# Kernel optimization log

Hardware: AMD Instinct MI355X
Metric: run time of the kernel (lower is better)

The kernel has to match this reference:

```python
import jax, jax.numpy as jnp
import numpy as np

NEG_SLOPE = 0.01  # torch F.leaky_relu default
EPS = 1e-5        # torch BatchNorm default
N_HEADS = 8


def _bn(x, g, b):
    # BatchNorm3d in training mode: batch statistics over (N, D, H, W)
    mu = jnp.mean(x, axis=(0, 2, 3, 4), keepdims=True)
    var = jnp.var(x, axis=(0, 2, 3, 4), keepdims=True)
    xn = (x - mu) * jax.lax.rsqrt(var + EPS)
    return xn * g[None, :, None, None, None] + b[None, :, None, None, None]


def _leaky(x):
    return jnp.where(x >= 0, x, NEG_SLOPE * x)


def setup_inputs() -> dict:
    key = jax.random.key(0)
    ks = jax.random.split(key, 6)
    B, C, T, X, Y = 4, 64, 8, 96, 96
    s = 0.02
    return {
        "h": jax.random.normal(ks[0], (B, C, T, X, Y), jnp.float32),
        "conv0_w": jax.random.normal(ks[1], (C, C, 1, 3, 3), jnp.float32) * s,
        "conv0_b": jnp.zeros((C,), jnp.float32),
        "bn0_g": jnp.ones((C,), jnp.float32),
        "bn0_b": jnp.zeros((C,), jnp.float32),
        "bn1_g": jnp.ones((C,), jnp.float32),
        "bn1_b": jnp.zeros((C,), jnp.float32),
        "in_proj_w": jax.random.normal(ks[2], (3 * C, C), jnp.float32) * s,
        "in_proj_b": jnp.zeros((3 * C,), jnp.float32),
        "out_proj_w": jax.random.normal(ks[3], (C, C), jnp.float32) * s,
        "out_proj_b": jnp.zeros((C,), jnp.float32),
        "conv1_w": jax.random.normal(ks[4], (25, C), jnp.float32) * s,  # Conv1d k=1, squeezed
        "conv1_b": jnp.zeros((25,), jnp.float32),
    }


def reference(h, conv0_w, conv0_b, bn0_g, bn0_b, bn1_g, bn1_b,
              in_proj_w, in_proj_b, out_proj_w, out_proj_b, conv1_w, conv1_b):
    B, C, T, X, Y = h.shape
    H = N_HEADS
    Dh = C // H
    h_in = h

    # conv0: Conv3d kernel [1,3,3], padding [0,1,1]
    x = jax.lax.conv_general_dilated(
        h, conv0_w, window_strides=(1, 1, 1),
        padding=[(0, 0), (1, 1), (1, 1)],
        dimension_numbers=("NCDHW", "OIDHW", "NCDHW"))
    x = x + conv0_b[None, :, None, None, None]
    x = _leaky(_bn(x, bn0_g, bn0_b))

    # self-attention over the T axis; batch = B*X*Y, embed = C (torch to_mha layout)
    seq = jnp.transpose(x, (2, 0, 3, 4, 1)).reshape(T, B * X * Y, C)  # [T, N, C]
    qkv = seq @ in_proj_w.T + in_proj_b
    q, k, v = jnp.split(qkv, 3, axis=-1)
    scale = 1.0 / np.sqrt(Dh)
    q = q.reshape(T, -1, H, Dh) * jnp.asarray(scale, q.dtype)
    k = k.reshape(T, -1, H, Dh)
    v = v.reshape(T, -1, H, Dh)
    attn = jax.nn.softmax(jnp.einsum("qnhd,knhd->nhqk", q, k), axis=-1)
    o = jnp.einsum("nhqk,knhd->qnhd", attn, v).reshape(T, -1, C)
    o = o @ out_proj_w.T + out_proj_b
    # from_mha: [T, B, X, Y, C] -> [B, C, T, X, Y]
    o = jnp.transpose(o.reshape(T, B, X, Y, C), (1, 4, 0, 2, 3))

    x = _leaky(_bn(x + o, bn1_g, bn1_b))

    # spatial mean + 1x1 Conv1d -> per-(b,t) 5x5 kernels
    m = jnp.mean(x, axis=(3, 4))                                   # [B, C, T]
    kern = jnp.einsum("bct,oc->bot", m, conv1_w) + conv1_b[None, :, None]  # [B, 25, T]
    w = jnp.transpose(kern, (0, 2, 1)).reshape(B * T, 1, 5, 5)

    # dynamic depthwise conv: each (b,t) kernel applied across all C slices of h_in
    lhs = jnp.transpose(h_in, (1, 0, 2, 3, 4)).reshape(C, B * T, X, Y)  # N=C, channels=B*T
    out = jax.lax.conv_general_dilated(
        lhs, w, window_strides=(1, 1), padding=[(2, 2), (2, 2)],
        dimension_numbers=("NCHW", "OIHW", "NCHW"),
        feature_group_count=B * T)
    out = jnp.transpose(out.reshape(C, B, T, X, Y), (1, 0, 2, 3, 4))
    return out
```

## Files before the change

### kernel.cpp

```cpp
#include <hip/hip_runtime.h>
#include <hip/hip_bf16.h>

typedef __attribute__((ext_vector_type(8))) short  short8;
typedef __attribute__((ext_vector_type(4))) short  short4v;
typedef __attribute__((ext_vector_type(4))) float  floatx4;
typedef unsigned short ushort_t;
typedef __attribute__((ext_vector_type(4))) unsigned short ushort4v;
typedef __attribute__((ext_vector_type(8))) unsigned short ushort8v;

constexpr int B_=4, C_=64, T_=8, X_=96, Y_=96;
constexpr int XY_  = X_*Y_;
constexpr int TOT_ = B_*C_*T_*XY_;
constexpr float EPS_   = 1e-5f;
constexpr float SLOPE_ = 0.01f;
constexpr float QSC_   = 0.35355339059327373f;
constexpr float INV_BN_ = 1.0f/294912.0f;
constexpr float INV_XY_ = 1.0f/9216.0f;

constexpr size_t OFF_HT   = 0;
constexpr size_t OFF_X0   = 37748736;
constexpr size_t OFF_X2   = OFF_X0 + (size_t)TOT_*2;
constexpr size_t OFF_WB   = OFF_X2 + (size_t)TOT_*2;
constexpr size_t OFF_QP   = OFF_WB + 73728;
constexpr size_t OFF_WP   = OFF_QP + 24576;
constexpr size_t OFF_SUM0 = OFF_WP + 8192;
constexpr size_t OFF_SQ0  = OFF_SUM0 + 256;
constexpr size_t OFF_SUM1 = OFF_SQ0 + 256;
constexpr size_t OFF_SQ1  = OFF_SUM1 + 256;
constexpr size_t OFF_M    = OFF_SQ1 + 256;
constexpr size_t ZBYTES   = 1024 + 8192;
constexpr size_t OFF_SC0  = OFF_M + 8192;
constexpr size_t OFF_SH0  = OFF_SC0 + 256;
constexpr size_t OFF_SC1  = OFF_SH0 + 256;
constexpr size_t OFF_SH1  = OFF_SC1 + 256;
constexpr size_t OFF_KERN = OFF_SH1 + 256;

__device__ __forceinline__ float leaky_(float v){ return v >= 0.f ? v : SLOPE_*v; }
__device__ __forceinline__ float bf2f(ushort_t u){
    union { unsigned int i; float f; } c; c.i = ((unsigned int)u) << 16; return c.f;
}
__device__ __forceinline__ ushort_t f2bf(float f){
    __hip_bfloat16 b = __float2bfloat16(f);
    return *reinterpret_cast<ushort_t*>(&b);
}
__device__ __forceinline__ void s8f(short8 s, float* f){
    union { short8 s; unsigned int u[4]; } c; c.s = s;
    #pragma unroll
    for (int i=0;i<4;++i){
        union { unsigned int i; float f; } lo, hi;
        lo.i = c.u[i] << 16; hi.i = c.u[i] & 0xffff0000u;
        f[2*i] = lo.f; f[2*i+1] = hi.f;
    }
}

__global__ void k_prep(const float* __restrict__ w0, const float* __restrict__ wqkv,
                       const float* __restrict__ wo,
                       ushort_t* __restrict__ wB, short* __restrict__ qP, short* __restrict__ wP){
    int i = blockIdx.x*256 + threadIdx.x;
    if (i < 36864){
        int j = i & 7, lane = (i>>3) & 63, frag = i >> 9;
        int nt = frag & 3, kb = (frag>>2) & 1, tap = frag >> 3;
        int co = nt*16 + (lane & 15);
        int ci = kb*32 + (lane>>4)*8 + j;
        wB[i] = f2bf(w0[co*576 + ci*9 + tap]);
    } else if (i < 49152){
        int pos = i - 36864;
        int j = pos & 7, lane = (pos>>3)&63, kb = (pos>>9)&1, nt = pos>>10;
        int n = nt*16 + (lane&15);
        int c = kb*32 + (lane>>4)*8 + j;
        qP[pos] = (short)f2bf(wqkv[n*64 + c]);
    } else if (i < 53248){
        int pos = i - 49152;
        int j = pos & 7, lane = (pos>>3)&63, kb = (pos>>9)&1, nt = pos>>10;
        int n = nt*16 + (lane&15);
        int c = kb*32 + (lane>>4)*8 + j;
        wP[pos] = (short)f2bf(wo[n*64 + c]);
    }
}

__global__ __launch_bounds__(256) void k_hT(const float* __restrict__ h,
                                            ushort_t* __restrict__ hT){
    __shared__ float s[96*65];
    int x = blockIdx.x, bt = blockIdx.y;
    int b = bt >> 3, t = bt & 7;
    int c = threadIdx.x >> 2, yq = threadIdx.x & 3;
    const float* hp = h + ((size_t)(b*64 + c)*8 + t)*9216 + x*96 + yq*24;
    #pragma unroll
    for (int i=0;i<6;i++){
        float4 v = *(const float4*)(hp + i*4);
        int y = yq*24 + i*4;
        s[(y+0)*65 + c] = v.x;
        s[(y+1)*65 + c] = v.y;
        s[(y+2)*65 + c] = v.z;
        s[(y+3)*65 + c] = v.w;
    }
    __syncthreads();
    ushort_t* op = hT + ((size_t)(bt*96 + x)*96)*64;
    int o0 = threadIdx.x*24;
    #pragma unroll
    for (int v8=0; v8<3; ++v8){
        ushort8v pk;
        #pragma unroll
        for (int j=0;j<8;j++){
            int o = o0 + v8*8 + j;
            pk[j] = f2bf(s[(o>>6)*65 + (o&63)]);
        }
        *(ushort8v*)(op + o0 + v8*8) = pk;
    }
}

__global__ __launch_bounds__(256) void k_conv0(const ushort_t* __restrict__ hT,
        const ushort_t* __restrict__ wB, const float* __restrict__ bias,
        ushort_t* __restrict__ x0, float* __restrict__ sum0, float* __restrict__ sq0){
    __shared__ float red[512];
    int tid = threadIdx.x;
    int lane = tid & 63, w = tid >> 6;
    int m = lane & 15, q = lane >> 4;
    int bt = blockIdx.y, b = bt >> 3, t = bt & 7;
    int xr = blockIdx.x*4 + w;
    floatx4 acc[6][4];
    #pragma unroll
    for (int nt=0; nt<4; ++nt){
        float bv = bias[nt*16 + m];
        #pragma unroll
        for (int mt=0; mt<6; ++mt) acc[mt][nt] = {bv,bv,bv,bv};
    }
    const ushort_t* hbase = hT + (size_t)bt*589824;
    #pragma unroll
    for (int tap=0; tap<9; ++tap){
        int dx = tap/3, dy = tap%3;
        int xx = xr + dx - 1;
        if ((unsigned)xx >= 96u) continue;
        const ushort_t* hrow = hbase + (size_t)xx*6144 + q*8;
        #pragma unroll
        for (int kb=0; kb<2; ++kb){
            short8 bf[4];
            #pragma unroll
            for (int nt=0; nt<4; ++nt)
                bf[nt] = *(const short8*)(wB + ((tap*2+kb)*4 + nt)*512 + lane*8);
            #pragma unroll
            for (int mt=0; mt<6; ++mt){
                int y = mt*16 + m + dy - 1;
                short8 a = {0,0,0,0,0,0,0,0};
                if ((unsigned)y < 96u)
                    a = *(const short8*)(hrow + y*64 + kb*32);
                #pragma unroll
                for (int nt=0; nt<4; ++nt)
                    acc[mt][nt] = __builtin_amdgcn_mfma_f32_16x16x32_bf16(a, bf[nt], acc[mt][nt], 0,0,0);
            }
        }
    }
    float ls[4] = {0,0,0,0}, lq[4] = {0,0,0,0};
    size_t outb = ((size_t)(b*9216 + xr*96)*8 + t)*64;
    #pragma unroll
    for (int mt=0; mt<6; ++mt){
        #pragma unroll
        for (int nt=0; nt<4; ++nt){
            #pragma unroll
            for (int r=0; r<4; ++r){
                float v = acc[mt][nt][r];
                ls[nt] += v; lq[nt] += v*v;
                int y = mt*16 + q*4 + r;
                x0[outb + (size_t)y*512 + nt*16 + m] = f2bf(v);
            }
        }
    }
    #pragma unroll
    for (int nt=0; nt<4; ++nt){
        ls[nt] += __shfl_xor(ls[nt], 16); ls[nt] += __shfl_xor(ls[nt], 32);
        lq[nt] += __shfl_xor(lq[nt], 16); lq[nt] += __shfl_xor(lq[nt], 32);
    }
    if (lane < 16){
        #pragma unroll
        for (int nt=0; nt<4; ++nt){
            red[w*64 + nt*16 + lane]       = ls[nt];
            red[256 + w*64 + nt*16 + lane] = lq[nt];
        }
    }
    __syncthreads();
    if (tid < 64){
        float a  = red[tid] + red[64+tid] + red[128+tid] + red[192+tid];
        float qq = red[256+tid] + red[320+tid] + red[384+tid] + red[448+tid];
        atomicAdd(&sum0[tid], a);
        atomicAdd(&sq0[tid], qq);
    }
}

__global__ void k_fin(const float* __restrict__ sum, const float* __restrict__ sq,
                      const float* __restrict__ g, const float* __restrict__ be,
                      float* __restrict__ scale, float* __restrict__ shift, float inv_n){
    int c = threadIdx.x;
    float mu = sum[c]*inv_n;
    float var = sq[c]*inv_n - mu*mu;
    float rs = rsqrtf(var + EPS_);
    float sc = g[c]*rs;
    scale[c] = sc; shift[c] = be[c] - mu*sc;
}

__device__ __forceinline__ void attn_one(ushort_t* qs, const float* qf, int tok, int p, int h){
    int off_k = 64  + ((h ^ p)<<3);
    int off_v = 128 + ((h ^ p)<<3);
    float sv[8]; float mx = -1e30f;
    #pragma unroll
    for (int kt=0; kt<8; ++kt){
        short8 kv = *(const short8*)(qs + (p*8+kt)*200 + off_k);
        float kf[8]; s8f(kv, kf);
        float s = qf[0]*kf[0]+qf[1]*kf[1]+qf[2]*kf[2]+qf[3]*kf[3]
                + qf[4]*kf[4]+qf[5]*kf[5]+qf[6]*kf[6]+qf[7]*kf[7];
        sv[kt] = s; mx = fmaxf(mx, s);
    }
    float ssum = 0.f;
    #pragma unroll
    for (int kt=0;kt<8;++kt){ sv[kt] = __expf(sv[kt]-mx); ssum += sv[kt]; }
    float inv = 1.f/ssum;
    float o[8] = {0,0,0,0,0,0,0,0};
    #pragma unroll
    for (int kt=0;kt<8;++kt){
        short8 vv = *(const short8*)(qs + (p*8+kt)*200 + off_v);
        float vf[8]; s8f(vv, vf);
        #pragma unroll
        for (int j=0;j<8;++j) o[j] += sv[kt]*vf[j];
    }
    short8 ov;
    #pragma unroll
    for (int j=0;j<8;++j) ov[j] = (short)f2bf(o[j]*inv);
    *(short8*)(qs + tok*200 + h*8) = ov;
}

__global__ __launch_bounds__(256, 3) void k_attn(const ushort_t* __restrict__ x0,
        const float* __restrict__ sc0, const float* __restrict__ sh0,
        const short* __restrict__ qP, const float* __restrict__ bqkv,
        const short* __restrict__ wP, const float* __restrict__ bo,
        ushort_t* __restrict__ x2, float* __restrict__ sum1, float* __restrict__ sq1){
    __shared__ __align__(16) char smem[51200];
    ushort_t* qsA = (ushort_t*)smem;
    ushort_t* qsB = (ushort_t*)(smem + 25600);

    int tid = threadIdx.x;
    int b = blockIdx.z, xx = blockIdx.y, y0 = blockIdx.x*16;
    size_t slabA = ((size_t)(b*9216 + xx*96 + y0)) * 512;
    size_t slabB = slabA + 4096;

    int lane = tid & 63, w = tid >> 6;
    int c16 = lane & 15, qd = lane >> 4;

    {
        int tokA = w*16 + c16;
        const ushort_t* xrA = x0 + slabA + (size_t)tokA*64;
        const ushort_t* xrB = x0 + slabB + (size_t)tokA*64;
        ushort8v xaA = *(const ushort8v*)(xrA + qd*8);
        ushort8v xbA = *(const ushort8v*)(xrA + 32 + qd*8);
        ushort8v xaB = *(const ushort8v*)(xrB + qd*8);
        ushort8v xbB = *(const ushort8v*)(xrB + 32 + qd*8);
        float sca[8], sha[8], scb[8], shb[8];
        #pragma unroll
        for (int j=0;j<8;++j){
            sca[j] = sc0[qd*8 + j];      sha[j] = sh0[qd*8 + j];
            scb[j] = sc0[32 + qd*8 + j]; shb[j] = sh0[32 + qd*8 + j];
        }
        short8 a0A, a1A, a0B, a1B;
        #pragma unroll
        for (int j=0;j<8;++j){
            a0A[j] = (short)f2bf(leaky_(bf2f(xaA[j])*sca[j] + sha[j]));
            a1A[j] = (short)f2bf(leaky_(bf2f(xbA[j])*scb[j] + shb[j]));
            a0B[j] = (short)f2bf(leaky_(bf2f(xaB[j])*sca[j] + sha[j]));
            a1B[j] = (short)f2bf(leaky_(bf2f(xbB[j])*scb[j] + shb[j]));
        }
        #pragma unroll
        for (int nt=0; nt<12; ++nt){
            float bv = bqkv[nt*16 + c16];
            short8 b0 = *(const short8*)(qP + (nt*2+0)*512 + lane*8);
            short8 b1 = *(const short8*)(qP + (nt*2+1)*512 + lane*8);
            floatx4 accA = {bv,bv,bv,bv};
            floatx4 accB = {bv,bv,bv,bv};
            accA = __builtin_amdgcn_mfma_f32_16x16x32_bf16(a0A, b0, accA, 0, 0, 0);
            accB = __builtin_amdgcn_mfma_f32_16x16x32_bf16(a0B, b0, accB, 0, 0, 0);
            accA = __builtin_amdgcn_mfma_f32_16x16x32_bf16(a1A, b1, accA, 0, 0, 0);
            accB = __builtin_amdgcn_mfma_f32_16x16x32_bf16(a1B, b1, accB, 0, 0, 0);
            if (nt < 4){
                #pragma unroll
                for (int r=0;r<4;++r){ accA[r]*=QSC_; accB[r]*=QSC_; }
            }
            int c8 = nt*2 + (c16>>3);
            int sub = c16 & 7;
            #pragma unroll
            for (int r=0;r<4;++r){
                int row = w*16 + qd*4 + r;
                int p = row >> 3;
                qsA[row*200 + ((c8 ^ p)<<3) + sub] = f2bf(accA[r]);
                qsB[row*200 + ((c8 ^ p)<<3) + sub] = f2bf(accB[r]);
            }
        }
    }
    __syncthreads();

    {
        int tok = lane, p = tok >> 3;
        float qA0[8], qA1[8], qB0[8], qB1[8];
        short8 t0 = *(const short8*)(qsA + tok*200 + (((w  ) ^ p)<<3));
        short8 t1 = *(const short8*)(qsA + tok*200 + (((w+4) ^ p)<<3));
        short8 t2 = *(const short8*)(qsB + tok*200 + (((w  ) ^ p)<<3));
        short8 t3 = *(const short8*)(qsB + tok*200 + (((w+4) ^ p)<<3));
        s8f(t0, qA0); s8f(t1, qA1); s8f(t2, qB0); s8f(t3, qB1);
        attn_one(qsA, qA0, tok, p, w);
        attn_one(qsB, qB0, tok, p, w);
        attn_one(qsA, qA1, tok, p, w+4);
        attn_one(qsB, qB1, tok, p, w+4);
    }
    __syncthreads();

    {
        int row3 = w*16 + c16;
        short8 A0A = *(const short8*)(qsA + row3*200 + qd*8);
        short8 A1A = *(const short8*)(qsA + row3*200 + 32 + qd*8);
        short8 A0B = *(const short8*)(qsB + row3*200 + qd*8);
        short8 A1B = *(const short8*)(qsB + row3*200 + 32 + qd*8);
        #pragma unroll
        for (int nt=0; nt<4; ++nt){
            float bv = bo[nt*16 + c16];
            short8 b0 = *(const short8*)(wP + (nt*2+0)*512 + lane*8);
            short8 b1 = *(const short8*)(wP + (nt*2+1)*512 + lane*8);
            floatx4 accA = {bv,bv,bv,bv};
            floatx4 accB = {bv,bv,bv,bv};
            accA = __builtin_amdgcn_mfma_f32_16x16x32_bf16(A0A, b0, accA, 0, 0, 0);
            accB = __builtin_amdgcn_mfma_f32_16x16x32_bf16(A0B, b0, accB, 0, 0, 0);
            accA = __builtin_amdgcn_mfma_f32_16x16x32_bf16(A1A, b1, accA, 0, 0, 0);
            accB = __builtin_amdgcn_mfma_f32_16x16x32_bf16(A1B, b1, accB, 0, 0, 0);
            #pragma unroll
            for (int r=0;r<4;++r){
                int row = w*16 + qd*4 + r;
                qsA[row*200 + 64 + nt*16 + c16] = f2bf(accA[r]);
                qsB[row*200 + 64 + nt*16 + c16] = f2bf(accB[r]);
            }
        }
    }
    __syncthreads();

    float ls[4] = {0,0,0,0}, lq[4] = {0,0,0,0};
    #pragma unroll
    for (int it=0; it<4; ++it){
        int g = tid + it*256;
        int e0 = g*4, tk = g>>4, c0 = e0 & 63;
        floatx4 sc = *(const floatx4*)(sc0 + c0);
        floatx4 sh = *(const floatx4*)(sh0 + c0);
        ushort4v xvA = *(const ushort4v*)(x0 + slabA + e0);
        ushort4v xvB = *(const ushort4v*)(x0 + slabB + e0);
        short4v ovA = *(const short4v*)(qsA + tk*200 + 64 + c0);
        short4v ovB = *(const short4v*)(qsB + tk*200 + 64 + c0);
        ushort4v stA, stB;
        #pragma unroll
        for (int j=0;j<4;++j){
            float x1A = leaky_(bf2f(xvA[j])*sc[j] + sh[j]);
            float x1B = leaky_(bf2f(xvB[j])*sc[j] + sh[j]);
            stA[j] = f2bf(x1A + bf2f((ushort_t)ovA[j]));
            stB[j] = f2bf(x1B + bf2f((ushort_t)ovB[j]));
            float vA = bf2f(stA[j]), vB = bf2f(stB[j]);
            ls[j] += vA + vB; lq[j] += vA*vA + vB*vB;
        }
        *(ushort4v*)(x2 + slabA + e0) = stA;
        *(ushort4v*)(x2 + slabB + e0) = stB;
    }
    __syncthreads();
    float* red = (float*)smem;
    int slot = tid >> 4, c0s = (tid*4) & 63;
    #pragma unroll
    for (int j=0;j<4;++j){
        red[slot*64 + c0s + j]        = ls[j];
        red[1024 + slot*64 + c0s + j] = lq[j];
    }
    __syncthreads();
    if (tid < 128){
        int c = tid & 63;
        const float* base = red + (tid>>6)*1024 + c;
        float a = 0.f;
        #pragma unroll
        for (int s=0;s<16;++s) a += base[s*64];
        atomicAdd((tid < 64) ? &sum1[c] : &sq1[c], a);
    }
}

__global__ __launch_bounds__(256) void k_m(const ushort_t* __restrict__ x2,
        const float* __restrict__ sc1, const float* __restrict__ sh1,
        float* __restrict__ msum){
    __shared__ float sred[2048];
    int c = threadIdx.x & 63, tg = threadIdx.x >> 6;
    int b = blockIdx.y, chunk = blockIdx.x;
    float macc[8] = {0,0,0,0,0,0,0,0};
    float sc = sc1[c], sh = sh1[c];
    int xy_end = chunk*96 + 96;
    for (int xy = chunk*96 + tg; xy < xy_end; xy += 4){
        size_t base = ((size_t)(b*9216 + xy)*8)*64 + c;
        #pragma unroll
        for (int t=0;t<8;t++){
            float v = bf2f(x2[base + (size_t)t*64]);
            macc[t] += leaky_(v*sc + sh);
        }
    }
    #pragma unroll
    for (int t=0;t<8;t++) sred[tg*512 + t*64 + c] = macc[t];
    __syncthreads();
    #pragma unroll
    for (int i=0;i<2;++i){
        int idx = threadIdx.x + i*256;
        float a = sred[idx] + sred[512+idx] + sred[1024+idx] + sred[1536+idx];
        atomicAdd(&msum[b*512 + idx], a);
    }
}

__global__ void k_kern(const float* __restrict__ msum, const float* __restrict__ w1,
                       const float* __restrict__ b1, float* __restrict__ kern){
    int tid = blockIdx.x*256 + threadIdx.x;
    if (tid >= 800) return;
    int o = tid % 25; int t = (tid/25) % 8; int b = tid/200;
    float s = b1[o];
    const float* mrow = msum + (b*8+t)*64;
    for (int c=0;c<64;c++) s += (mrow[c]*INV_XY_) * w1[o*64+c];
    kern[(b*8+t)*25 + o] = s;
}

__global__ __launch_bounds__(256) void k_final(const float* __restrict__ h,
        const float* __restrict__ kern, float* __restrict__ out){
    __shared__ float s[100*104];
    int bct = blockIdx.x;
    int b = bct >> 9, t = bct & 7;
    int tid = threadIdx.x;
    const float* hp = h + (size_t)bct*9216;
    for (int i = tid; i < 1184; i += 256){
        int row, col;
        if (i < 416){ int r4 = i/104; row = (r4<2) ? r4 : 96 + r4; col = i - r4*104; }
        else { int j = i - 416; row = 2 + (j>>3); int k = j & 7; col = (k<4) ? k : 96 + k; }
        s[row*104 + col] = 0.f;
    }
    for (int i = tid; i < 2304; i += 256){
        int e = i*4; int xx = e/96, yy = e%96;
        float4 v = *(const float4*)(hp + e);
        *(float4*)(&s[(xx+2)*104 + yy + 4]) = v;
    }
    const float* kp = kern + ((size_t)(b*8+t))*25;
    float kv[25];
    #pragma unroll
    for (int i=0;i<25;i++) kv[i] = kp[i];
    __syncthreads();
    int tx = tid & 15, ty = tid >> 4;
    int x0 = ty*6, y0 = tx*6;
    float acc[6][6];
    #pragma unroll
    for (int i=0;i<6;i++)
        #pragma unroll
        for (int j=0;j<6;j++) acc[i][j] = 0.f;
    #pragma unroll
    for (int r=0; r<10; ++r){
        float row[10];
        const float* sp = &s[(x0+r)*104 + y0 + 2];
        #pragma unroll
        for (int c=0;c<10;c++) row[c] = sp[c];
        #pragma unroll
        for (int orow=0; orow<6; ++orow){
            if (orow > r || orow < r-4) continue;
            int dx = r - orow;
            #pragma unroll
            for (int dy=0; dy<5; ++dy){
                float wv = kv[dx*5+dy];
                #pragma unroll
                for (int oc=0; oc<6; ++oc)
                    acc[orow][oc] += wv * row[oc+dy];
            }
        }
    }
    float* op = out + (size_t)bct*9216 + x0*96 + y0;
    #pragma unroll
    for (int orow=0; orow<6; ++orow)
        #pragma unroll
        for (int oc=0; oc<6; ++oc)
            op[orow*96 + oc] = acc[orow][oc];
}

extern "C" void kernel_launch(void* const* d_in, const int* in_sizes, int n_in,
                              void* d_out, int out_size, void* d_ws, size_t ws_size,
                              hipStream_t stream){
    const float* h    = (const float*)d_in[0];
    const float* w0   = (const float*)d_in[1];
    const float* cb0  = (const float*)d_in[2];
    const float* bn0g = (const float*)d_in[3];
    const float* bn0b = (const float*)d_in[4];
    const float* bn1g = (const float*)d_in[5];
    const float* bn1b = (const float*)d_in[6];
    const float* wqkv = (const float*)d_in[7];
    const float* bqkv = (const float*)d_in[8];
    const float* wo   = (const float*)d_in[9];
    const float* bo   = (const float*)d_in[10];
    const float* w1   = (const float*)d_in[11];
    const float* b1   = (const float*)d_in[12];

    char* ws = (char*)d_ws;
    ushort_t* hT  = (ushort_t*)(ws + OFF_HT);
    ushort_t* x0  = (ushort_t*)(ws + OFF_X0);
    ushort_t* x2  = (ushort_t*)(ws + OFF_X2);
    ushort_t* wB  = (ushort_t*)(ws + OFF_WB);
    short* qP     = (short*)(ws + OFF_QP);
    short* wP     = (short*)(ws + OFF_WP);
    float* sum0   = (float*)(ws + OFF_SUM0);
    float* sq0    = (float*)(ws + OFF_SQ0);
    float* sum1   = (float*)(ws + OFF_SUM1);
    float* sq1    = (float*)(ws + OFF_SQ1);
    float* msum   = (float*)(ws + OFF_M);
    float* sc0    = (float*)(ws + OFF_SC0);
    float* sh0    = (float*)(ws + OFF_SH0);
    float* sc1    = (float*)(ws + OFF_SC1);
    float* sh1    = (float*)(ws + OFF_SH1);
    float* kern   = (float*)(ws + OFF_KERN);
    float* outp   = (float*)d_out;

    hipMemsetAsync(ws + OFF_SUM0, 0, ZBYTES, stream);
    k_prep  <<<208, 256, 0, stream>>>(w0, wqkv, wo, wB, qP, wP);
    k_hT    <<<dim3(96, 32), 256, 0, stream>>>(h, hT);
    k_conv0 <<<dim3(24, 32), 256, 0, stream>>>(hT, wB, cb0, x0, sum0, sq0);
    k_fin   <<<1, 64, 0, stream>>>(sum0, sq0, bn0g, bn0b, sc0, sh0, INV_BN_);
    k_attn  <<<dim3(6, 96, 4), 256, 0, stream>>>(x0, sc0, sh0, qP, bqkv, wP, bo, x2, sum1, sq1);
    k_fin   <<<1, 64, 0, stream>>>(sum1, sq1, bn1g, bn1b, sc1, sh1, INV_BN_);
    k_m     <<<dim3(96, 4), 256, 0, stream>>>(x2, sc1, sh1, msum);
    k_kern  <<<4, 256, 0, stream>>>(msum, w1, b1, kern);
    k_final <<<2048, 256, 0, stream>>>(h, kern, outp);
}
```

Measured before the change: 357.4 us.

## Pad hT rows with zero halo and split conv0 across y halves

The transposed bf16 input buffer gains a zero row at each end of every y line, so conv0 can drop its per-load y-bounds checks. conv0 now splits the 96 y positions into two halves via blockIdx.z, which halves its accumulator count and doubles the grid. It also adds a launch-bounds occupancy hint. The aim is more waves in flight and less branching in the MFMA loop, at the cost of a slightly larger hT buffer and x-tap loads repeated across both halves.

```diff
diff --git a/kernel.cpp b/kernel.cpp
--- a/kernel.cpp
+++ b/kernel.cpp
@@ -17,8 +17,13 @@
 constexpr float INV_BN_ = 1.0f/294912.0f;
 constexpr float INV_XY_ = 1.0f/9216.0f;
 
+constexpr int HT_ROWS_ = 98;
+constexpr int HT_XSTR_ = HT_ROWS_*64;
+constexpr int HT_BTSTR_ = 96*HT_XSTR_;
+constexpr size_t HT_BYTES_ = (size_t)32*HT_BTSTR_*2;
+
 constexpr size_t OFF_HT   = 0;
-constexpr size_t OFF_X0   = 37748736;
+constexpr size_t OFF_X0   = HT_BYTES_;
 constexpr size_t OFF_X2   = OFF_X0 + (size_t)TOT_*2;
 constexpr size_t OFF_WB   = OFF_X2 + (size_t)TOT_*2;
 constexpr size_t OFF_QP   = OFF_WB + 73728;
@@ -95,7 +100,14 @@
         s[(y+3)*65 + c] = v.w;
     }
     __syncthreads();
-    ushort_t* op = hT + ((size_t)(bt*96 + x)*96)*64;
+    ushort_t* opb = hT + (size_t)(bt*96 + x)*HT_XSTR_;
+    if (threadIdx.x < 16){
+        ushort8v z8 = {0,0,0,0,0,0,0,0};
+        int r = (threadIdx.x < 8) ? 0 : 97;
+        int o = (threadIdx.x & 7)*8;
+        *(ushort8v*)(opb + r*64 + o) = z8;
+    }
+    ushort_t* op = opb + 64;
     int o0 = threadIdx.x*24;
     #pragma unroll
     for (int v8=0; v8<3; ++v8){
@@ -109,7 +121,7 @@
     }
 }
 
-__global__ __launch_bounds__(256) void k_conv0(const ushort_t* __restrict__ hT,
+__global__ __launch_bounds__(256, 5) void k_conv0(const ushort_t* __restrict__ hT,
         const ushort_t* __restrict__ wB, const float* __restrict__ bias,
         ushort_t* __restrict__ x0, float* __restrict__ sum0, float* __restrict__ sq0){
     __shared__ float red[512];
@@ -118,20 +130,21 @@
     int m = lane & 15, q = lane >> 4;
     int bt = blockIdx.y, b = bt >> 3, t = bt & 7;
     int xr = blockIdx.x*4 + w;
-    floatx4 acc[6][4];
+    int z = blockIdx.z;
+    floatx4 acc[3][4];
     #pragma unroll
     for (int nt=0; nt<4; ++nt){
         float bv = bias[nt*16 + m];
         #pragma unroll
-        for (int mt=0; mt<6; ++mt) acc[mt][nt] = {bv,bv,bv,bv};
-    }
-    const ushort_t* hbase = hT + (size_t)bt*589824;
+        for (int mt=0; mt<3; ++mt) acc[mt][nt] = {bv,bv,bv,bv};
+    }
+    const ushort_t* hbase = hT + (size_t)bt*HT_BTSTR_;
     #pragma unroll
     for (int tap=0; tap<9; ++tap){
         int dx = tap/3, dy = tap%3;
         int xx = xr + dx - 1;
         if ((unsigned)xx >= 96u) continue;
-        const ushort_t* hrow = hbase + (size_t)xx*6144 + q*8;
+        const ushort_t* hrow = hbase + (size_t)xx*HT_XSTR_ + (z*48 + m + dy)*64 + q*8;
         #pragma unroll
         for (int kb=0; kb<2; ++kb){
             short8 bf[4];
@@ -139,11 +152,8 @@
             for (int nt=0; nt<4; ++nt)
                 bf[nt] = *(const short8*)(wB + ((tap*2+kb)*4 + nt)*512 + lane*8);
             #pragma unroll
-            for (int mt=0; mt<6; ++mt){
-                int y = mt*16 + m + dy - 1;
-                short8 a = {0,0,0,0,0,0,0,0};
-                if ((unsigned)y < 96u)
-                    a = *(const short8*)(hrow + y*64 + kb*32);
+            for (int mt=0; mt<3; ++mt){
+                short8 a = *(const short8*)(hrow + mt*1024 + kb*32);
                 #pragma unroll
                 for (int nt=0; nt<4; ++nt)
                     acc[mt][nt] = __builtin_amdgcn_mfma_f32_16x16x32_bf16(a, bf[nt], acc[mt][nt], 0,0,0);
@@ -153,14 +163,14 @@
     float ls[4] = {0,0,0,0}, lq[4] = {0,0,0,0};
     size_t outb = ((size_t)(b*9216 + xr*96)*8 + t)*64;
     #pragma unroll
-    for (int mt=0; mt<6; ++mt){
+    for (int mt=0; mt<3; ++mt){
         #pragma unroll
         for (int nt=0; nt<4; ++nt){
             #pragma unroll
             for (int r=0; r<4; ++r){
                 float v = acc[mt][nt][r];
                 ls[nt] += v; lq[nt] += v*v;
-                int y = mt*16 + q*4 + r;
+                int y = z*48 + mt*16 + q*4 + r;
                 x0[outb + (size_t)y*512 + nt*16 + m] = f2bf(v);
             }
         }
@@ -514,7 +524,7 @@
     hipMemsetAsync(ws + OFF_SUM0, 0, ZBYTES, stream);
     k_prep  <<<208, 256, 0, stream>>>(w0, wqkv, wo, wB, qP, wP);
     k_hT    <<<dim3(96, 32), 256, 0, stream>>>(h, hT);
-    k_conv0 <<<dim3(24, 32), 256, 0, stream>>>(hT, wB, cb0, x0, sum0, sq0);
+    k_conv0 <<<dim3(24, 32, 2), 256, 0, stream>>>(hT, wB, cb0, x0, sum0, sq0);
     k_fin   <<<1, 64, 0, stream>>>(sum0, sq0, bn0g, bn0b, sc0, sh0, INV_BN_);
     k_attn  <<<dim3(6, 96, 4), 256, 0, stream>>>(x0, sc0, sh0, qP, bqkv, wP, bo, x2, sum1, sq1);
     k_fin   <<<1, 64, 0, stream>>>(sum1, sq1, bn1g, bn1b, sc1, sh1, INV_BN_);
```

After: 367.1 us. 1.03x slower.

## Stage padded hT tile into LDS for conv0 with swizzled async loads

Applied to the files above, without the earlier changes.

The transposed input hT is now stored with a one-row, one-column zero halo (98x98 per bt), so conv0 no longer needs bounds checks. Each conv0 block copies its 6-row padded tile into LDS with global_load_lds and an XOR swizzle, then reads the A fragments for all nine taps from LDS instead of re-reading global memory. This is meant to cut redundant global and L2 traffic across taps. The cost is about 76KB of LDS per block, which limits occupancy to 2 blocks per CU, plus extra halo writes in k_hT.

```diff
diff --git a/kernel.cpp b/kernel.cpp
--- a/kernel.cpp
+++ b/kernel.cpp
@@ -17,8 +17,12 @@
 constexpr float INV_BN_ = 1.0f/294912.0f;
 constexpr float INV_XY_ = 1.0f/9216.0f;
 
+constexpr int HT_XSTR_  = 98*64;
+constexpr int HT_BTSTR_ = 98*HT_XSTR_;
+constexpr size_t HT_BYTES_ = (size_t)32*HT_BTSTR_*2;
+
 constexpr size_t OFF_HT   = 0;
-constexpr size_t OFF_X0   = 37748736;
+constexpr size_t OFF_X0   = HT_BYTES_ + 4096;
 constexpr size_t OFF_X2   = OFF_X0 + (size_t)TOT_*2;
 constexpr size_t OFF_WB   = OFF_X2 + (size_t)TOT_*2;
 constexpr size_t OFF_QP   = OFF_WB + 73728;
@@ -51,6 +55,11 @@
         lo.i = c.u[i] << 16; hi.i = c.u[i] & 0xffff0000u;
         f[2*i] = lo.f; f[2*i+1] = hi.f;
     }
+}
+__device__ __forceinline__ void gld16(const void* gp, void* lp){
+    __builtin_amdgcn_global_load_lds(
+        (const __attribute__((address_space(1))) void*)gp,
+        (__attribute__((address_space(3))) void*)lp, 16, 0, 0);
 }
 
 __global__ void k_prep(const float* __restrict__ w0, const float* __restrict__ wqkv,
@@ -81,8 +90,16 @@
 __global__ __launch_bounds__(256) void k_hT(const float* __restrict__ h,
                                             ushort_t* __restrict__ hT){
     __shared__ float s[96*65];
-    int x = blockIdx.x, bt = blockIdx.y;
+    int xp = blockIdx.x, bt = blockIdx.y;
     int b = bt >> 3, t = bt & 7;
+    ushort_t* opb = hT + (size_t)(bt*98 + xp)*HT_XSTR_;
+    if (xp == 0 || xp == 97){
+        ushort8v z8 = {0,0,0,0,0,0,0,0};
+        for (int i = threadIdx.x; i < 784; i += 256)
+            *(ushort8v*)(opb + i*8) = z8;
+        return;
+    }
+    int x = xp - 1;
     int c = threadIdx.x >> 2, yq = threadIdx.x & 3;
     const float* hp = h + ((size_t)(b*64 + c)*8 + t)*9216 + x*96 + yq*24;
     #pragma unroll
@@ -95,7 +112,13 @@
         s[(y+3)*65 + c] = v.w;
     }
     __syncthreads();
-    ushort_t* op = hT + ((size_t)(bt*96 + x)*96)*64;
+    if (threadIdx.x < 16){
+        ushort8v z8 = {0,0,0,0,0,0,0,0};
+        int r = (threadIdx.x < 8) ? 0 : 97;
+        int o = (threadIdx.x & 7)*8;
+        *(ushort8v*)(opb + r*64 + o) = z8;
+    }
+    ushort_t* op = opb + 64;
     int o0 = threadIdx.x*24;
     #pragma unroll
     for (int v8=0; v8<3; ++v8){
@@ -109,15 +132,27 @@
     }
 }
 
-__global__ __launch_bounds__(256) void k_conv0(const ushort_t* __restrict__ hT,
+__global__ __launch_bounds__(256, 2) void k_conv0(const ushort_t* __restrict__ hT,
         const ushort_t* __restrict__ wB, const float* __restrict__ bias,
         ushort_t* __restrict__ x0, float* __restrict__ sum0, float* __restrict__ sq0){
+    __shared__ __align__(16) char lds[77824];
     __shared__ float red[512];
     int tid = threadIdx.x;
     int lane = tid & 63, w = tid >> 6;
     int m = lane & 15, q = lane >> 4;
     int bt = blockIdx.y, b = bt >> 3, t = bt & 7;
-    int xr = blockIdx.x*4 + w;
+    int bx = blockIdx.x;
+    int xr = bx*4 + w;
+
+    {
+        const char* gsrc = (const char*)(hT + ((size_t)bt*98 + bx*4)*HT_XSTR_);
+        #pragma unroll
+        for (int it=0; it<19; ++it){
+            int lin = (tid + it*256)*16;
+            int src = lin ^ (((lin>>7)&7)<<4);
+            gld16(gsrc + src, lds + lin);
+        }
+    }
     floatx4 acc[6][4];
     #pragma unroll
     for (int nt=0; nt<4; ++nt){
@@ -125,25 +160,23 @@
         #pragma unroll
         for (int mt=0; mt<6; ++mt) acc[mt][nt] = {bv,bv,bv,bv};
     }
-    const ushort_t* hbase = hT + (size_t)bt*589824;
+    __syncthreads();
+
     #pragma unroll
     for (int tap=0; tap<9; ++tap){
-        int dx = tap/3, dy = tap%3;
-        int xx = xr + dx - 1;
-        if ((unsigned)xx >= 96u) continue;
-        const ushort_t* hrow = hbase + (size_t)xx*6144 + q*8;
+        const int dx = tap/3, dy = tap%3;
+        int rowg = (w + dx)*98 + m + dy;
+        int swz  = (rowg & 7) << 4;
         #pragma unroll
         for (int kb=0; kb<2; ++kb){
             short8 bf[4];
             #pragma unroll
             for (int nt=0; nt<4; ++nt)
                 bf[nt] = *(const short8*)(wB + ((tap*2+kb)*4 + nt)*512 + lane*8);
+            int va = (rowg*128 + kb*64 + q*16) ^ swz;
             #pragma unroll
             for (int mt=0; mt<6; ++mt){
-                int y = mt*16 + m + dy - 1;
-                short8 a = {0,0,0,0,0,0,0,0};
-                if ((unsigned)y < 96u)
-                    a = *(const short8*)(hrow + y*64 + kb*32);
+                short8 a = *(const short8*)(lds + va + mt*2048);
                 #pragma unroll
                 for (int nt=0; nt<4; ++nt)
                     acc[mt][nt] = __builtin_amdgcn_mfma_f32_16x16x32_bf16(a, bf[nt], acc[mt][nt], 0,0,0);
@@ -513,7 +546,7 @@
 
     hipMemsetAsync(ws + OFF_SUM0, 0, ZBYTES, stream);
     k_prep  <<<208, 256, 0, stream>>>(w0, wqkv, wo, wB, qP, wP);
-    k_hT    <<<dim3(96, 32), 256, 0, stream>>>(h, hT);
+    k_hT    <<<dim3(98, 32), 256, 0, stream>>>(h, hT);
     k_conv0 <<<dim3(24, 32), 256, 0, stream>>>(hT, wB, cb0, x0, sum0, sq0);
     k_fin   <<<1, 64, 0, stream>>>(sum0, sq0, bn0g, bn0b, sc0, sh0, INV_BN_);
     k_attn  <<<dim3(6, 96, 4), 256, 0, stream>>>(x0, sc0, sh0, qP, bqkv, wP, bo, x2, sum1, sq1);
```

After: 327.5 us. 1.09x faster.
